# Performance work log

Hardware: AMD Instinct MI355X
Metric: run time of the kernel (lower is better)

Reference implementation:

```python
import jax, jax.numpy as jnp
import numpy as np

D_MODEL = 1024
NUM_HEADS = 16
DEPTH = D_MODEL // NUM_HEADS
B, S = 4, 2048


def setup_inputs() -> dict:
    key = jax.random.key(0)
    ks = jax.random.split(key, 12)
    s = 1.0 / np.sqrt(D_MODEL)
    return {
        "q": jax.random.normal(ks[0], (B, S, D_MODEL), jnp.float32),
        "k": jax.random.normal(ks[1], (B, S, D_MODEL), jnp.float32),
        "v": jax.random.normal(ks[2], (B, S, D_MODEL), jnp.float32),
        "mask": jax.random.randint(ks[3], (B, S), 0, 2, jnp.int32),
        "wq_w": jax.random.uniform(ks[4], (D_MODEL, D_MODEL), jnp.float32, -s, s),
        "wq_b": jnp.zeros((D_MODEL,), jnp.float32),
        "wk_w": jax.random.uniform(ks[5], (D_MODEL, D_MODEL), jnp.float32, -s, s),
        "wk_b": jnp.zeros((D_MODEL,), jnp.float32),
        "wv_w": jax.random.uniform(ks[6], (D_MODEL, D_MODEL), jnp.float32, -s, s),
        "wv_b": jnp.zeros((D_MODEL,), jnp.float32),
        "wo_w": jax.random.uniform(ks[7], (D_MODEL, D_MODEL), jnp.float32, -s, s),
        "wo_b": jnp.zeros((D_MODEL,), jnp.float32),
    }


def _split_heads(x):
    # [B, S, D] -> [B, H, S, depth]
    b, s, _ = x.shape
    return x.reshape(b, s, NUM_HEADS, DEPTH).transpose(0, 2, 1, 3)


def reference(q, k, v, mask, wq_w, wq_b, wk_w, wk_b, wv_w, wv_b, wo_w, wo_b):
    qh = _split_heads(q @ wq_w.T + wq_b)
    kh = _split_heads(k @ wk_w.T + wk_b)
    vh = _split_heads(v @ wv_w.T + wv_b)
    # [B, H, Sq, Sk]
    logits = jnp.einsum("bhqd,bhkd->bhqk", qh, kh) / jnp.sqrt(
        jnp.asarray(DEPTH, jnp.float32))
    # 2D mask -> [B, 1, 1, Sk], masked_fill where mask == 0
    m = mask[:, None, None, :]
    logits = jnp.where(m == 0, jnp.asarray(-1e9, logits.dtype), logits)
    attn = jax.nn.softmax(logits, axis=-1)
    out = jnp.einsum("bhqk,bhkd->bhqd", attn, vh)
    out = out.transpose(0, 2, 1, 3).reshape(q.shape[0], -1, D_MODEL)
    return out @ wo_w.T + wo_b
```

## Files before the change

### kernel.cpp

```cpp
#include <hip/hip_runtime.h>
#include <hip/hip_bf16.h>
#include <stdint.h>

typedef __bf16 bf16_t;
typedef __bf16 bf16x8 __attribute__((ext_vector_type(8)));
typedef __bf16 bf16x2 __attribute__((ext_vector_type(2)));
typedef float  f32x4  __attribute__((ext_vector_type(4)));
typedef float  f32x16 __attribute__((ext_vector_type(16)));
typedef unsigned int u32;
typedef u32 u32x4 __attribute__((ext_vector_type(4)));

#define D_MODEL 1024
#define NHEAD   16
#define DEPTH   64
#define BATCH   4
#define SEQ     2048
#define MROWS   (BATCH*SEQ)

#define SC 0.18033688011112042f

__device__ __forceinline__ void gload16(const void* g, void* l) {
    __builtin_amdgcn_global_load_lds(
        (__attribute__((address_space(1))) void*)(uintptr_t)g,
        (__attribute__((address_space(3))) void*)l,
        16, 0, 0);
}

__device__ __forceinline__ u32 pk2(float a, float b) {
    bf16x2 t; t[0] = (bf16_t)a; t[1] = (bf16_t)b;
    return __builtin_bit_cast(u32, t);
}

__global__ __launch_bounds__(256) void cvt_kernel(const float* __restrict__ src,
                                                  bf16_t* __restrict__ dst, int n8) {
    int i = blockIdx.x * 256 + threadIdx.x;
    if (i >= n8) return;
    const float4* s4 = (const float4*)src;
    float4 a = s4[2*(size_t)i], b = s4[2*(size_t)i + 1];
    bf16x8 o;
    o[0] = (bf16_t)a.x; o[1] = (bf16_t)a.y; o[2] = (bf16_t)a.z; o[3] = (bf16_t)a.w;
    o[4] = (bf16_t)b.x; o[5] = (bf16_t)b.y; o[6] = (bf16_t)b.z; o[7] = (bf16_t)b.w;
    *(bf16x8*)(dst + 8*(size_t)i) = o;
}

__global__ __launch_bounds__(256) void cvtw_kernel(const float* __restrict__ s0, bf16_t* __restrict__ d0,
                                                   const float* __restrict__ s1, bf16_t* __restrict__ d1,
                                                   const float* __restrict__ s2, bf16_t* __restrict__ d2,
                                                   const float* __restrict__ s3, bf16_t* __restrict__ d3,
                                                   int n8) {
    int i = blockIdx.x * 256 + threadIdx.x;
    if (i >= n8) return;
    const float* src; bf16_t* dst;
    switch (blockIdx.y) {
        case 0: src = s0; dst = d0; break;
        case 1: src = s1; dst = d1; break;
        case 2: src = s2; dst = d2; break;
        default: src = s3; dst = d3; break;
    }
    const float4* s4 = (const float4*)src;
    float4 a = s4[2*(size_t)i], b = s4[2*(size_t)i + 1];
    bf16x8 o;
    o[0] = (bf16_t)a.x; o[1] = (bf16_t)a.y; o[2] = (bf16_t)a.z; o[3] = (bf16_t)a.w;
    o[4] = (bf16_t)b.x; o[5] = (bf16_t)b.y; o[6] = (bf16_t)b.z; o[7] = (bf16_t)b.w;
    *(bf16x8*)(dst + 8*(size_t)i) = o;
}

__global__ __launch_bounds__(256) void vtrans_kernel(const bf16_t* __restrict__ Vp,
                                                     bf16_t* __restrict__ Vt) {
    __shared__ bf16_t T[64][257];
    const int bh = blockIdx.y;
    const int b = bh >> 4, h = bh & 15;
    const int s0 = blockIdx.x * 256;
    const int tid = threadIdx.x;
#pragma unroll
    for (int p = 0; p < 8; ++p) {
        int id = p*256 + tid;
        int sl = id >> 3, dg = id & 7;
        bf16x8 v = *(const bf16x8*)&Vp[((size_t)b*SEQ + s0 + sl)*D_MODEL + h*DEPTH + dg*8];
#pragma unroll
        for (int e = 0; e < 8; ++e) T[dg*8 + e][sl] = v[e];
    }
    __syncthreads();
#pragma unroll
    for (int p = 0; p < 8; ++p) {
        int id = p*256 + tid;
        int d = id >> 5, sg = id & 31;
        bf16x8 o;
#pragma unroll
        for (int e = 0; e < 8; ++e) {
            int sp = sg*8 + e;
            int s  = (sp & ~12) | ((sp & 4) << 1) | ((sp & 8) >> 1);
            o[e] = T[d][s];
        }
        *(bf16x8*)&Vt[((size_t)bh*DEPTH + d)*SEQ + s0 + sg*8] = o;
    }
}

template<int OUT_BF16>
__global__ __launch_bounds__(256) void gemm_bt(const bf16_t* __restrict__ A,
                                               const bf16_t* __restrict__ Bw,
                                               const float* __restrict__ bias,
                                               bf16_t* __restrict__ Cb,
                                               float* __restrict__ Cf,
                                               int M, int N, int K, float scale) {
    __shared__ bf16_t As[128*64];
    __shared__ bf16_t Bs[128*64];
    const int tid  = threadIdx.x;
    const int wave = tid >> 6, lane = tid & 63;
    const int lr = lane & 15, lk = (lane >> 4) * 8;
    const int bm = blockIdx.x * 128, bn = blockIdx.y * 128;
    const int wr = (wave >> 1) * 64, wc = (wave & 1) * 64;

    f32x4 acc[4][4] = {};

    for (int kt = 0; kt < K; kt += 64) {
#pragma unroll
        for (int p = 0; p < 4; ++p) {
            int chunk = p*256 + tid;
            int r  = chunk >> 3;
            int cs = ((chunk & 7) ^ (r & 7)) * 8;
            gload16(A  + (size_t)(bm + r)*K + kt + cs, As + (size_t)(p*256 + wave*64)*8);
            gload16(Bw + (size_t)(bn + r)*K + kt + cs, Bs + (size_t)(p*256 + wave*64)*8);
        }
        __syncthreads();
        const char* AsB = (const char*)As;
        const char* BsB = (const char*)Bs;
#pragma unroll
        for (int ks = 0; ks < 2; ++ks) {
            int kb = (ks*32 + lk) * 2;
            bf16x8 af[4], bfv[4];
#pragma unroll
            for (int mi = 0; mi < 4; ++mi) {
                int row = wr + mi*16 + lr;
                af[mi] = *(const bf16x8*)(AsB + ((row*128 + kb) ^ ((row & 7) << 4)));
            }
#pragma unroll
            for (int ni = 0; ni < 4; ++ni) {
                int row = wc + ni*16 + lr;
                bfv[ni] = *(const bf16x8*)(BsB + ((row*128 + kb) ^ ((row & 7) << 4)));
            }
            __builtin_amdgcn_s_setprio(1);
#pragma unroll
            for (int mi = 0; mi < 4; ++mi)
#pragma unroll
                for (int ni = 0; ni < 4; ++ni)
                    acc[mi][ni] = __builtin_amdgcn_mfma_f32_16x16x32_bf16(
                        af[mi], bfv[ni], acc[mi][ni], 0, 0, 0);
            __builtin_amdgcn_s_setprio(0);
        }
        __syncthreads();
    }

#pragma unroll
    for (int ni = 0; ni < 4; ++ni) {
        int col = bn + wc + ni*16 + lr;
        float bv = bias[col];
#pragma unroll
        for (int mi = 0; mi < 4; ++mi) {
#pragma unroll
            for (int j = 0; j < 4; ++j) {
                int row = bm + wr + mi*16 + (lane >> 4)*4 + j;
                float vv = (acc[mi][ni][j] + bv) * scale;
                if (OUT_BF16) Cb[(size_t)row*N + col] = (bf16_t)vv;
                else          Cf[(size_t)row*N + col] = vv;
            }
        }
    }
}

__global__ __launch_bounds__(256, 3) void attn_kernel(const bf16_t* __restrict__ Qp,
                                                      const bf16_t* __restrict__ Kp,
                                                      const bf16_t* __restrict__ Vt,
                                                      const int* __restrict__ mask,
                                                      bf16_t* __restrict__ AO) {
    __shared__ bf16_t Ks[3][64*64];
    __shared__ bf16_t Vs[3][64*64];
    __shared__ bf16_t mbias[SEQ];

    const int tid  = threadIdx.x;
    const int wave = tid >> 6, lane = tid & 63;
    const int lr5 = lane & 31;
    const int hi  = lane >> 5;

    const int flat = blockIdx.x + 16*blockIdx.y + 256*blockIdx.z;
    const int xcd = flat & 7, slot = flat >> 3;
    const int bh = xcd + 8*(slot >> 4);
    const int b = bh >> 4, h = bh & 15;
    const int q0 = (slot & 15) * 128;

    const int qw = q0 + wave*32;
    const size_t base  = (size_t)b * SEQ * D_MODEL + (size_t)h * DEPTH;
    const size_t vbase = (size_t)bh * DEPTH * SEQ;

    bf16x8 qf[4];
#pragma unroll
    for (int dc = 0; dc < 4; ++dc)
        qf[dc] = *(const bf16x8*)&Qp[base + (size_t)(qw + lr5)*D_MODEL + dc*16 + hi*8];

    u32x4 onew = {};
    onew[0] = hi ? 0u : 0x3F80u;
    const bf16x8 qone = __builtin_bit_cast(bf16x8, onew);

    {
        const int4* mp = (const int4*)&mask[(size_t)b*SEQ + tid*8];
        int4 m0 = mp[0], m1 = mp[1];
        bf16x8 mm;
        mm[0] = (m0.x == 0) ? (bf16_t)(-1e30f) : (bf16_t)0.0f;
        mm[1] = (m0.y == 0) ? (bf16_t)(-1e30f) : (bf16_t)0.0f;
        mm[2] = (m0.z == 0) ? (bf16_t)(-1e30f) : (bf16_t)0.0f;
        mm[3] = (m0.w == 0) ? (bf16_t)(-1e30f) : (bf16_t)0.0f;
        mm[4] = (m1.x == 0) ? (bf16_t)(-1e30f) : (bf16_t)0.0f;
        mm[5] = (m1.y == 0) ? (bf16_t)(-1e30f) : (bf16_t)0.0f;
        mm[6] = (m1.z == 0) ? (bf16_t)(-1e30f) : (bf16_t)0.0f;
        mm[7] = (m1.w == 0) ? (bf16_t)(-1e30f) : (bf16_t)0.0f;
        *(bf16x8*)&mbias[tid*8] = mm;
    }

    auto stage = [&](int t, int buf) {
#pragma unroll
        for (int p = 0; p < 2; ++p) {
            int chunk = p*256 + tid; int r = chunk >> 3;
            int cs = ((chunk & 7) ^ (r & 7)) * 8;
            gload16(Kp + base + (size_t)(t*64 + r)*D_MODEL + cs,
                    (bf16_t*)Ks[buf] + (size_t)chunk*8);
            gload16(Vt + vbase + (size_t)r*SEQ + t*64 + cs,
                    (bf16_t*)Vs[buf] + (size_t)chunk*8);
        }
    };

    f32x16 o0 = {}, o1 = {};
    float l_run = 0.f;

    stage(0, 0); stage(1, 1); stage(2, 2);
    asm volatile("s_waitcnt vmcnt(4) lgkmcnt(0)");
    __builtin_amdgcn_s_barrier();

    int cb = 0;
    for (int t = 0; t < SEQ/64; ++t) {
        u32 mw0 = (u32)__builtin_bit_cast(unsigned short, mbias[t*64 + lr5]);
        u32 mw1 = (u32)__builtin_bit_cast(unsigned short, mbias[t*64 + 32 + lr5]);
        if (hi) { mw0 = 0; mw1 = 0; }
        u32x4 mv0 = {}, mv1 = {};
        mv0[0] = mw0; mv1[0] = mw1;
        bf16x8 afm0 = __builtin_bit_cast(bf16x8, mv0);
        bf16x8 afm1 = __builtin_bit_cast(bf16x8, mv1);

        const char* KsB = (const char*)Ks[cb];
        const f32x16 zz = {};
        f32x16 s0, s1;
        __builtin_amdgcn_s_setprio(1);
        s0 = __builtin_amdgcn_mfma_f32_32x32x16_bf16(afm0, qone, zz, 0, 0, 0);
        s1 = __builtin_amdgcn_mfma_f32_32x32x16_bf16(afm1, qone, zz, 0, 0, 0);
#pragma unroll
        for (int dc = 0; dc < 4; ++dc) {
            int colb = dc*32 + hi*16;
            int row0 = lr5, row1 = 32 + lr5;
            bf16x8 kf0 = *(const bf16x8*)(KsB + ((row0*128 + colb) ^ ((row0 & 7) << 4)));
            bf16x8 kf1 = *(const bf16x8*)(KsB + ((row1*128 + colb) ^ ((row1 & 7) << 4)));
            s0 = __builtin_amdgcn_mfma_f32_32x32x16_bf16(kf0, qf[dc], s0, 0, 0, 0);
            s1 = __builtin_amdgcn_mfma_f32_32x32x16_bf16(kf1, qf[dc], s1, 0, 0, 0);
        }
        __builtin_amdgcn_s_setprio(0);

        const char* VsB = (const char*)Vs[cb];
#pragma unroll
        for (int kt = 0; kt < 2; ++kt) {
            const f32x16& sh = kt ? s1 : s0;
            float pv[16];
#pragma unroll
            for (int r = 0; r < 16; ++r) pv[r] = __builtin_exp2f(sh[r]);
            float su0 = 0.f, su1 = 0.f, su2 = 0.f, su3 = 0.f;
#pragma unroll
            for (int r = 0; r < 16; r += 4) {
                su0 += pv[r]; su1 += pv[r+1]; su2 += pv[r+2]; su3 += pv[r+3];
            }
            l_run += (su0 + su1) + (su2 + su3);
#pragma unroll
            for (int c = 0; c < 2; ++c) {
                u32x4 fwv;
#pragma unroll
                for (int i = 0; i < 4; ++i)
                    fwv[i] = pk2(pv[c*8 + 2*i], pv[c*8 + 2*i + 1]);
                bf16x8 pfrag = __builtin_bit_cast(bf16x8, fwv);
                int colb = kt*64 + c*32 + hi*16;
                int row0 = lr5, row1 = 32 + lr5;
                bf16x8 vf0 = *(const bf16x8*)(VsB + ((row0*128 + colb) ^ ((row0 & 7) << 4)));
                bf16x8 vf1 = *(const bf16x8*)(VsB + ((row1*128 + colb) ^ ((row1 & 7) << 4)));
                __builtin_amdgcn_s_setprio(1);
                o0 = __builtin_amdgcn_mfma_f32_32x32x16_bf16(vf0, pfrag, o0, 0, 0, 0);
                o1 = __builtin_amdgcn_mfma_f32_32x32x16_bf16(vf1, pfrag, o1, 0, 0, 0);
                __builtin_amdgcn_s_setprio(0);
            }
        }

        asm volatile("s_waitcnt vmcnt(0)");
        __builtin_amdgcn_s_barrier();
        if (t + 3 < SEQ/64) stage(t + 3, cb);
        ++cb; if (cb == 3) cb = 0;
    }

    float l_tot = l_run + __shfl_xor(l_run, 32);
    float inv = 1.f / l_tot;
    char* TrB = (char*)Ks;
    const int qloc = wave*32 + lr5;
#pragma unroll
    for (int mt = 0; mt < 2; ++mt)
#pragma unroll
        for (int r = 0; r < 16; ++r) {
            int d = mt*32 + (r & 3) + 8*(r >> 2) + 4*hi;
            float val = (mt ? o1[r] : o0[r]) * inv;
            *(bf16_t*)(TrB + (qloc*128 + ((d*2) ^ ((qloc & 7) << 4)))) = (bf16_t)val;
        }
    __syncthreads();
#pragma unroll
    for (int p = 0; p < 4; ++p) {
        int id = p*256 + tid;
        int row = id >> 3, g = id & 7;
        bf16x8 v8 = *(const bf16x8*)(TrB + (row*128 + ((g*16) ^ ((row & 7) << 4))));
        *(bf16x8*)&AO[base + (size_t)(q0 + row)*D_MODEL + g*8] = v8;
    }
}

extern "C" void kernel_launch(void* const* d_in, const int* in_sizes, int n_in,
                              void* d_out, int out_size, void* d_ws, size_t ws_size,
                              hipStream_t stream) {
    (void)in_sizes; (void)n_in; (void)out_size; (void)ws_size;
    const float* q    = (const float*)d_in[0];
    const float* k    = (const float*)d_in[1];
    const float* v    = (const float*)d_in[2];
    const int*   mask = (const int*)d_in[3];
    const float* wq_w = (const float*)d_in[4];
    const float* wq_b = (const float*)d_in[5];
    const float* wk_w = (const float*)d_in[6];
    const float* wk_b = (const float*)d_in[7];
    const float* wv_w = (const float*)d_in[8];
    const float* wv_b = (const float*)d_in[9];
    const float* wo_w = (const float*)d_in[10];
    const float* wo_b = (const float*)d_in[11];
    float* out = (float*)d_out;

    const size_t ACT = (size_t)MROWS * D_MODEL;
    const size_t WSZ = (size_t)D_MODEL * D_MODEL;
    bf16_t* Xb = (bf16_t*)d_ws;
    bf16_t* Qp = Xb + ACT;
    bf16_t* Kp = Qp + ACT;
    bf16_t* Vp = Kp + ACT;
    bf16_t* Wq = Vp + ACT;
    bf16_t* Wk = Wq + WSZ;
    bf16_t* Wv = Wk + WSZ;
    bf16_t* Wo = Wv + WSZ;
    bf16_t* Vt = Xb;
    bf16_t* AO = Vp;

    const int wn8 = (int)(WSZ/8), an8 = (int)(ACT/8);
    cvtw_kernel<<<dim3(wn8/256, 4), dim3(256), 0, stream>>>(wq_w, Wq, wk_w, Wk, wv_w, Wv, wo_w, Wo, wn8);

    dim3 ggrid(MROWS/128, D_MODEL/128);
    cvt_kernel<<<dim3(an8/256), dim3(256), 0, stream>>>(q, Xb, an8);
    gemm_bt<1><<<ggrid, dim3(256), 0, stream>>>(Xb, Wq, wq_b, Qp, nullptr, MROWS, D_MODEL, D_MODEL, SC);
    cvt_kernel<<<dim3(an8/256), dim3(256), 0, stream>>>(k, Xb, an8);
    gemm_bt<1><<<ggrid, dim3(256), 0, stream>>>(Xb, Wk, wk_b, Kp, nullptr, MROWS, D_MODEL, D_MODEL, 1.f);
    cvt_kernel<<<dim3(an8/256), dim3(256), 0, stream>>>(v, Xb, an8);
    gemm_bt<1><<<ggrid, dim3(256), 0, stream>>>(Xb, Wv, wv_b, Vp, nullptr, MROWS, D_MODEL, D_MODEL, 1.f);

    vtrans_kernel<<<dim3(SEQ/256, NHEAD*BATCH), dim3(256), 0, stream>>>(Vp, Vt);

    attn_kernel<<<dim3(SEQ/128, NHEAD, BATCH), dim3(256), 0, stream>>>(Qp, Kp, Vt, mask, AO);

    gemm_bt<0><<<ggrid, dim3(256), 0, stream>>>(AO, Wo, wo_b, nullptr, out, MROWS, D_MODEL, D_MODEL, 1.f);
}
```

Before: 238.1 us.

## Fuse V transpose into V-projection GEMM epilogue and compute row sums via MFMA

The V projection GEMM gains a mode that writes its output through shared memory, directly in the transposed, permuted per-head layout attention expects. This removes the separate vtrans kernel launch and its extra global read/write pass over V. In the attention kernel, the softmax denominator is now accumulated with an extra MFMA against a ones fragment instead of scalar adds, and the pipeline waitcnts are relaxed so outstanding loads can overlap across iterations. The extra MFMA adds matrix work per tile, and the looser vmcnt depends on the exact count of loads each stage issues.

```diff
diff --git a/kernel.cpp b/kernel.cpp
--- a/kernel.cpp
+++ b/kernel.cpp
@@ -65,46 +65,16 @@
     *(bf16x8*)(dst + 8*(size_t)i) = o;
 }
 
-__global__ __launch_bounds__(256) void vtrans_kernel(const bf16_t* __restrict__ Vp,
-                                                     bf16_t* __restrict__ Vt) {
-    __shared__ bf16_t T[64][257];
-    const int bh = blockIdx.y;
-    const int b = bh >> 4, h = bh & 15;
-    const int s0 = blockIdx.x * 256;
-    const int tid = threadIdx.x;
-#pragma unroll
-    for (int p = 0; p < 8; ++p) {
-        int id = p*256 + tid;
-        int sl = id >> 3, dg = id & 7;
-        bf16x8 v = *(const bf16x8*)&Vp[((size_t)b*SEQ + s0 + sl)*D_MODEL + h*DEPTH + dg*8];
-#pragma unroll
-        for (int e = 0; e < 8; ++e) T[dg*8 + e][sl] = v[e];
-    }
-    __syncthreads();
-#pragma unroll
-    for (int p = 0; p < 8; ++p) {
-        int id = p*256 + tid;
-        int d = id >> 5, sg = id & 31;
-        bf16x8 o;
-#pragma unroll
-        for (int e = 0; e < 8; ++e) {
-            int sp = sg*8 + e;
-            int s  = (sp & ~12) | ((sp & 4) << 1) | ((sp & 8) >> 1);
-            o[e] = T[d][s];
-        }
-        *(bf16x8*)&Vt[((size_t)bh*DEPTH + d)*SEQ + s0 + sg*8] = o;
-    }
-}
-
-template<int OUT_BF16>
+template<int MODE>
 __global__ __launch_bounds__(256) void gemm_bt(const bf16_t* __restrict__ A,
                                                const bf16_t* __restrict__ Bw,
                                                const float* __restrict__ bias,
                                                bf16_t* __restrict__ Cb,
                                                float* __restrict__ Cf,
                                                int M, int N, int K, float scale) {
-    __shared__ bf16_t As[128*64];
-    __shared__ bf16_t Bs[128*64];
+    __shared__ bf16_t Smem[2*128*64];
+    bf16_t* As = Smem;
+    bf16_t* Bs = Smem + 128*64;
     const int tid  = threadIdx.x;
     const int wave = tid >> 6, lane = tid & 63;
     const int lr = lane & 15, lk = (lane >> 4) * 8;
@@ -151,19 +121,49 @@
         __syncthreads();
     }
 
-#pragma unroll
-    for (int ni = 0; ni < 4; ++ni) {
-        int col = bn + wc + ni*16 + lr;
-        float bv = bias[col];
-#pragma unroll
-        for (int mi = 0; mi < 4; ++mi) {
-#pragma unroll
-            for (int j = 0; j < 4; ++j) {
-                int row = bm + wr + mi*16 + (lane >> 4)*4 + j;
-                float vv = (acc[mi][ni][j] + bv) * scale;
-                if (OUT_BF16) Cb[(size_t)row*N + col] = (bf16_t)vv;
-                else          Cf[(size_t)row*N + col] = vv;
+    if (MODE != 2) {
+#pragma unroll
+        for (int ni = 0; ni < 4; ++ni) {
+            int col = bn + wc + ni*16 + lr;
+            float bv = bias[col];
+#pragma unroll
+            for (int mi = 0; mi < 4; ++mi) {
+#pragma unroll
+                for (int j = 0; j < 4; ++j) {
+                    int row = bm + wr + mi*16 + (lane >> 4)*4 + j;
+                    float vv = (acc[mi][ni][j] + bv) * scale;
+                    if (MODE == 1) Cb[(size_t)row*N + col] = (bf16_t)vv;
+                    else           Cf[(size_t)row*N + col] = vv;
+                }
             }
+        }
+    } else {
+        char* TB = (char*)Smem;
+#pragma unroll
+        for (int ni = 0; ni < 4; ++ni) {
+            int col = wc + ni*16 + lr;
+            int swz = (col & 7) << 4;
+            float bv = bias[bn + col];
+#pragma unroll
+            for (int mi = 0; mi < 4; ++mi)
+#pragma unroll
+                for (int j = 0; j < 4; ++j) {
+                    int row = wr + mi*16 + (lane >> 4)*4 + j;
+                    int sp  = (row & ~12) | ((row & 4) << 1) | ((row & 8) >> 1);
+                    float vv = (acc[mi][ni][j] + bv) * scale;
+                    *(bf16_t*)(TB + ((col*256 + sp*2) ^ swz)) = (bf16_t)vv;
+                }
+        }
+        __syncthreads();
+        const int b = bm >> 11, sl = bm & 2047;
+#pragma unroll
+        for (int p = 0; p < 8; ++p) {
+            int id = p*256 + tid;
+            int col = id >> 4, sg = id & 15;
+            bf16x8 v8 = *(const bf16x8*)(TB + ((col*256 + sg*16) ^ ((col & 7) << 4)));
+            int gc = bn + col;
+            int bh = b*16 + (gc >> 6), d = gc & 63;
+            *(bf16x8*)&Cb[((size_t)bh*DEPTH + d)*SEQ + sl + sg*8] = v8;
         }
     }
 }
@@ -200,6 +200,11 @@
     u32x4 onew = {};
     onew[0] = hi ? 0u : 0x3F80u;
     const bf16x8 qone = __builtin_bit_cast(bf16x8, onew);
+
+    u32x4 lonesw = {};
+    if (lr5 == 0) { lonesw[0] = 0x3F803F80u; lonesw[1] = 0x3F803F80u;
+                    lonesw[2] = 0x3F803F80u; lonesw[3] = 0x3F803F80u; }
+    const bf16x8 onesA = __builtin_bit_cast(bf16x8, lonesw);
 
     {
         const int4* mp = (const int4*)&mask[(size_t)b*SEQ + tid*8];
@@ -229,10 +234,10 @@
     };
 
     f32x16 o0 = {}, o1 = {};
-    float l_run = 0.f;
+    f32x16 l_acc = {};
 
     stage(0, 0); stage(1, 1); stage(2, 2);
-    asm volatile("s_waitcnt vmcnt(4) lgkmcnt(0)");
+    asm volatile("s_waitcnt vmcnt(8) lgkmcnt(0)");
     __builtin_amdgcn_s_barrier();
 
     int cb = 0;
@@ -269,12 +274,6 @@
             float pv[16];
 #pragma unroll
             for (int r = 0; r < 16; ++r) pv[r] = __builtin_exp2f(sh[r]);
-            float su0 = 0.f, su1 = 0.f, su2 = 0.f, su3 = 0.f;
-#pragma unroll
-            for (int r = 0; r < 16; r += 4) {
-                su0 += pv[r]; su1 += pv[r+1]; su2 += pv[r+2]; su3 += pv[r+3];
-            }
-            l_run += (su0 + su1) + (su2 + su3);
 #pragma unroll
             for (int c = 0; c < 2; ++c) {
                 u32x4 fwv;
@@ -289,17 +288,18 @@
                 __builtin_amdgcn_s_setprio(1);
                 o0 = __builtin_amdgcn_mfma_f32_32x32x16_bf16(vf0, pfrag, o0, 0, 0, 0);
                 o1 = __builtin_amdgcn_mfma_f32_32x32x16_bf16(vf1, pfrag, o1, 0, 0, 0);
+                l_acc = __builtin_amdgcn_mfma_f32_32x32x16_bf16(onesA, pfrag, l_acc, 0, 0, 0);
                 __builtin_amdgcn_s_setprio(0);
             }
         }
 
-        asm volatile("s_waitcnt vmcnt(0)");
+        asm volatile("s_waitcnt vmcnt(4) lgkmcnt(0)");
         __builtin_amdgcn_s_barrier();
         if (t + 3 < SEQ/64) stage(t + 3, cb);
         ++cb; if (cb == 3) cb = 0;
     }
 
-    float l_tot = l_run + __shfl_xor(l_run, 32);
+    float l_tot = l_acc[0] + __shfl_xor(l_acc[0], 32);
     float inv = 1.f / l_tot;
     char* TrB = (char*)Ks;
     const int qloc = wave*32 + lr5;
@@ -344,13 +344,12 @@
     bf16_t* Xb = (bf16_t*)d_ws;
     bf16_t* Qp = Xb + ACT;
     bf16_t* Kp = Qp + ACT;
-    bf16_t* Vp = Kp + ACT;
-    bf16_t* Wq = Vp + ACT;
+    bf16_t* Vt = Kp + ACT;
+    bf16_t* Wq = Vt + ACT;
     bf16_t* Wk = Wq + WSZ;
     bf16_t* Wv = Wk + WSZ;
     bf16_t* Wo = Wv + WSZ;
-    bf16_t* Vt = Xb;
-    bf16_t* AO = Vp;
+    bf16_t* AO = Xb;
 
     const int wn8 = (int)(WSZ/8), an8 = (int)(ACT/8);
     cvtw_kernel<<<dim3(wn8/256, 4), dim3(256), 0, stream>>>(wq_w, Wq, wk_w, Wk, wv_w, Wv, wo_w, Wo, wn8);
@@ -361,9 +360,7 @@
     cvt_kernel<<<dim3(an8/256), dim3(256), 0, stream>>>(k, Xb, an8);
     gemm_bt<1><<<ggrid, dim3(256), 0, stream>>>(Xb, Wk, wk_b, Kp, nullptr, MROWS, D_MODEL, D_MODEL, 1.f);
     cvt_kernel<<<dim3(an8/256), dim3(256), 0, stream>>>(v, Xb, an8);
-    gemm_bt<1><<<ggrid, dim3(256), 0, stream>>>(Xb, Wv, wv_b, Vp, nullptr, MROWS, D_MODEL, D_MODEL, 1.f);
-
-    vtrans_kernel<<<dim3(SEQ/256, NHEAD*BATCH), dim3(256), 0, stream>>>(Vp, Vt);
+    gemm_bt<2><<<ggrid, dim3(256), 0, stream>>>(Xb, Wv, wv_b, Vt, nullptr, MROWS, D_MODEL, D_MODEL, 1.f);
 
     attn_kernel<<<dim3(SEQ/128, NHEAD, BATCH), dim3(256), 0, stream>>>(Qp, Kp, Vt, mask, AO);
 
```

New measurement: 243.1 us. 2.1% more time.
